# Optimization experiments

Hardware: AMD Instinct MI355X
Metric: run time of the kernel (lower is better)

The kernel has to match this reference:

```python
import jax, jax.numpy as jnp
import numpy as np

B, S, N, HID = 4, 512, 128, 64


def setup_inputs() -> dict:
    key = jax.random.key(0)
    ks = jax.random.split(key, 32)
    def rn(k, shape, scale=0.1):
        return jax.random.normal(k, shape, dtype=jnp.float32) * scale
    adj = jax.random.randint(ks[0], (N, N), 0, 2).astype(jnp.int32)
    adj = adj.at[jnp.arange(N), jnp.arange(N)].set(1)  # self loops
    inp = {
        'x': jax.random.normal(ks[1], (B, S, N, 1), dtype=jnp.float32),
        'adj': adj,
        'emb_w': rn(ks[2], (1, 16)), 'emb_b': jnp.zeros((16,), jnp.float32),
        'gat1_W': rn(ks[3], (16, 16)), 'gat1_a': rn(ks[4], (32, 1)),
        'gat2_W': rn(ks[5], (16, 8)), 'gat2_a': rn(ks[6], (16, 1)),
        'Wih0': rn(ks[7], (4 * HID, N)), 'Whh0': rn(ks[8], (4 * HID, HID)),
        'bih0': jnp.zeros((4 * HID,), jnp.float32), 'bhh0': jnp.zeros((4 * HID,), jnp.float32),
        'Wih1': rn(ks[9], (4 * HID, HID)), 'Whh1': rn(ks[10], (4 * HID, HID)),
        'bih1': jnp.zeros((4 * HID,), jnp.float32), 'bhh1': jnp.zeros((4 * HID,), jnp.float32),
    }
    comb = HID + 8 * N
    for i, name in enumerate(['dir', 'ret', 'vol']):
        o = 2 if name == 'vol' else 1
        inp[name + '_w1'] = rn(ks[11 + 4 * i], (comb, 32))
        inp[name + '_b1'] = jnp.zeros((32,), jnp.float32)
        inp[name + '_w2'] = rn(ks[12 + 4 * i], (32, o))
        inp[name + '_b2'] = jnp.zeros((o,), jnp.float32)
    return inp


def _gat(h, W, a, mask):
    # e_ij = leakyrelu(a1 . Wh_i + a2 . Wh_j): avoid torch's [M,N,N,2F] concat.
    Wh = h @ W                                  # [M, N, F]
    Fo = W.shape[1]
    f1 = Wh @ a[:Fo]                            # [M, N, 1]
    f2 = Wh @ a[Fo:]                            # [M, N, 1]
    e = jax.nn.leaky_relu(f1 + jnp.swapaxes(f2, 1, 2), 0.2)  # [M, N, N]
    e = jnp.where(mask, e, jnp.float32(-9e15))
    attn = jax.nn.softmax(e, axis=2)
    return attn @ Wh                            # [M, N, F]


def _lstm_layer(xs, Wih, Whh, bih, bhh):
    # xs: [S, B, I]; PyTorch gate order i, f, g, o
    Bsz = xs.shape[1]
    Hd = Whh.shape[1]
    def step(carry, xt):
        h, c = carry
        g = xt @ Wih.T + h @ Whh.T + bih + bhh
        i, f, gg, o = jnp.split(g, 4, axis=-1)
        c = jax.nn.sigmoid(f) * c + jax.nn.sigmoid(i) * jnp.tanh(gg)
        h = jax.nn.sigmoid(o) * jnp.tanh(c)
        return (h, c), h
    init = (jnp.zeros((Bsz, Hd), xs.dtype), jnp.zeros((Bsz, Hd), xs.dtype))
    _, hs = jax.lax.scan(step, init, xs)
    return hs


def reference(x, adj, emb_w, emb_b, gat1_W, gat1_a, gat2_W, gat2_a,
              Wih0, Whh0, bih0, bhh0, Wih1, Whh1, bih1, bhh1,
              dir_w1, dir_b1, dir_w2, dir_b2,
              ret_w1, ret_b1, ret_w2, ret_b2,
              vol_w1, vol_b1, vol_w2, vol_b2):
    Bz, Sz, Nz, _ = x.shape
    mask = (adj > 0)[None]                      # [1, N, N], broadcast over B*S
    xe = (x @ emb_w + emb_b).reshape(Bz * Sz, Nz, 16)
    xg = jax.nn.elu(_gat(xe, gat1_W, gat1_a, mask))   # gat1 concat=True -> elu
    xg = _gat(xg, gat2_W, gat2_a, mask)               # gat2 concat=False
    xg_out = xg.reshape(Bz, Sz, Nz * 8)[:, -1, :]
    xs = jnp.swapaxes(x.reshape(Bz, Sz, Nz), 0, 1)    # [S, B, N]
    hs = _lstm_layer(xs, Wih0, Whh0, bih0, bhh0)
    hs = _lstm_layer(hs, Wih1, Whh1, bih1, bhh1)      # inter-layer dropout off (eval)
    xl_out = hs[-1]                                   # [B, 64]
    c = jnp.concatenate([xl_out, xg_out], axis=1)     # [B, 64 + 8N]
    def head(w1, b1, w2, b2):
        return jax.nn.relu(c @ w1 + b1) @ w2 + b2
    return (head(dir_w1, dir_b1, dir_w2, dir_b2),
            head(ret_w1, ret_b1, ret_w2, ret_b2),
            head(vol_w1, vol_b1, vol_w2, vol_b2))
```

## Files before the change

kernel.cpp:

```cpp
#include <hip/hip_runtime.h>

#define SEQ   512
#define BATCH 4
#define NN    128
#define HID   64
#define G4    256
#define MAGIC 0x13579BDF

__device__ __forceinline__ float frcp(float x)  { return __builtin_amdgcn_rcpf(x); }
__device__ __forceinline__ float fsigm(float x) { return frcp(1.f + __expf(-x)); }
__device__ __forceinline__ float ftanh(float x) { return 1.f - 2.f * frcp(1.f + __expf(2.f * x)); }
__device__ __forceinline__ float lrelu(float x) { return x > 0.f ? x : 0.2f * x; }
__device__ __forceinline__ float dot4f(float4 w, float4 h) {
  return fmaf(w.x, h.x, fmaf(w.y, h.y, fmaf(w.z, h.z, w.w * h.w)));
}
__device__ __forceinline__ void pin4(float4& v) {
  asm volatile("" : "+v"(v.x), "+v"(v.y), "+v"(v.z), "+v"(v.w));
}
__device__ __forceinline__ float qsum(float x) {
  x += __int_as_float(__builtin_amdgcn_update_dpp(
      0, __float_as_int(x), 0xB1, 0xF, 0xF, true));
  x += __int_as_float(__builtin_amdgcn_update_dpp(
      0, __float_as_int(x), 0x4E, 0xF, 0xF, true));
  return x;
}
__device__ __forceinline__ float dotacc(const float4* w, const float4* h, float a) {
#pragma unroll
  for (int c = 0; c < 4; ++c) {
    a = fmaf(w[c].x, h[c].x, a);
    a = fmaf(w[c].y, h[c].y, a);
    a = fmaf(w[c].z, h[c].z, a);
    a = fmaf(w[c].w, h[c].w, a);
  }
  return a;
}

#define BAR_LDS() asm volatile("s_waitcnt lgkmcnt(0)\n\ts_barrier" ::: "memory")

__global__ __attribute__((amdgpu_flat_work_group_size(768, 768),
                          amdgpu_waves_per_eu(3, 3)))
void fused_all(
    const float* __restrict__ x, const int* __restrict__ adj,
    const float* __restrict__ emb_w, const float* __restrict__ emb_b,
    const float* __restrict__ W1, const float* __restrict__ a1,
    const float* __restrict__ W2, const float* __restrict__ a2,
    const float* __restrict__ Wih0, const float* __restrict__ Whh0,
    const float* __restrict__ bih0, const float* __restrict__ bhh0,
    const float* __restrict__ Wih1, const float* __restrict__ Whh1,
    const float* __restrict__ bih1, const float* __restrict__ bhh1,
    const float* __restrict__ dw1, const float* __restrict__ db1,
    const float* __restrict__ dw2, const float* __restrict__ db2,
    const float* __restrict__ rw1, const float* __restrict__ rb1,
    const float* __restrict__ rw2, const float* __restrict__ rb2,
    const float* __restrict__ vw1, const float* __restrict__ vb1,
    const float* __restrict__ vw2, const float* __restrict__ vb2,
    float* __restrict__ X0T, float* __restrict__ xg,
    int* __restrict__ flags, float* __restrict__ out)
{
  const int bid = blockIdx.x;
  const int tid = threadIdx.x;

  if (bid >= 4) {
    const int c = bid - 4;
    __shared__ __align__(16) float xls[NN];
    {
      const int g = tid >> 1, half = tid & 1;
      float4 w4[16];
      if (tid < 512) {
        const float4* wp = reinterpret_cast<const float4*>(Wih0 + g * NN + half * 64);
#pragma unroll
        for (int i = 0; i < 16; ++i) w4[i] = wp[i];
#pragma unroll
        for (int i = 0; i < 16; ++i) pin4(w4[i]);
      }
      const float bsum = (tid < 512) ? (bih0[g] + bhh0[g]) : 0.f;
      for (int phase = 0; phase < 4; ++phase) {
        const int T = c + 128 * phase;
        for (int bb = 0; bb < BATCH; ++bb) {
          if (tid < NN) xls[tid] = x[(bb * SEQ + T) * NN + tid];
          __syncthreads();
          if (tid < 512) {
            const float4* hp = reinterpret_cast<const float4*>(&xls[half * 64]);
            float p0 = 0.f, p1 = 0.f, p2 = 0.f, p3 = 0.f;
#pragma unroll
            for (int k = 0; k < 16; k += 4) {
              p0 += dot4f(w4[k],     hp[k]);
              p1 += dot4f(w4[k + 1], hp[k + 1]);
              p2 += dot4f(w4[k + 2], hp[k + 2]);
              p3 += dot4f(w4[k + 3], hp[k + 3]);
            }
            float p = (p0 + p1) + (p2 + p3);
            p += __shfl_xor(p, 1);
            if (half == 0)
              X0T[(4 * T + bb) * G4 + (g & 63) * 4 + (g >> 6)] = p + bsum;
          }
          __syncthreads();
        }
        if (tid == 0 && phase == 0)
          __hip_atomic_store(&flags[c], MAGIC, __ATOMIC_RELEASE,
                             __HIP_MEMORY_SCOPE_AGENT);
        if (tid == 0 && phase == 3)
          __hip_atomic_store(&flags[128 + c], MAGIC, __ATOMIC_RELEASE,
                             __HIP_MEMORY_SCOPE_AGENT);
      }
    }
    if (bid >= 8) return;

    const int b = bid - 4;
    __shared__ float adjm[NN * 129];
    __shared__ __align__(16) float gxls[NN];
    __shared__ float u[16], v[16];
    __shared__ float Wh2[NN][9];
    __shared__ float f1b[NN], f2b[NN];
    __shared__ float p[NN];

    for (int idx = tid; idx < NN * NN; idx += 768)
      adjm[(idx >> 7) * 129 + (idx & 127)] = (adj[idx] > 0) ? 1.f : 0.f;
    if (tid < NN) gxls[tid] = x[(b * SEQ + (SEQ - 1)) * NN + tid];
    if (tid < 16) {
      float uu = 0.f, vv = 0.f;
      for (int fp = 0; fp < 16; ++fp) {
        uu += emb_w[fp] * W1[fp * 16 + tid];
        vv += emb_b[fp] * W1[fp * 16 + tid];
      }
      u[tid] = uu; v[tid] = vv;
    }
    __syncthreads();
    float s1 = 0.f, t1 = 0.f, s2 = 0.f, t2 = 0.f;
    for (int f = 0; f < 16; ++f) {
      s1 += u[f] * a1[f];      t1 += v[f] * a1[f];
      s2 += u[f] * a1[16 + f]; t2 += v[f] * a1[16 + f];
    }
    if (tid < NN) {
      const int i = tid;
      const float f1i = gxls[i] * s1 + t1;
      float m = -1e30f;
      for (int j = 0; j < NN; ++j)
        if (adjm[i * 129 + j] != 0.f)
          m = fmaxf(m, lrelu(f1i + gxls[j] * s2 + t2));
      float ssum = 0.f, ps = 0.f;
      for (int j = 0; j < NN; ++j)
        if (adjm[i * 129 + j] != 0.f) {
          const float wgt = __expf(lrelu(f1i + gxls[j] * s2 + t2) - m);
          ssum += wgt; ps += wgt * gxls[j];
        }
      p[i] = ps / ssum;
    }
    __syncthreads();
    if (tid < NN) {
      const int i = tid;
      float xg1[16];
#pragma unroll
      for (int f = 0; f < 16; ++f) {
        const float ov = p[i] * u[f] + v[f];
        xg1[f] = ov > 0.f ? ov : expm1f(ov);
      }
      float wrow[8];
#pragma unroll
      for (int f2 = 0; f2 < 8; ++f2) wrow[f2] = 0.f;
#pragma unroll
      for (int f = 0; f < 16; ++f) {
        const float xv = xg1[f];
#pragma unroll
        for (int f2 = 0; f2 < 8; ++f2) wrow[f2] += xv * W2[f * 8 + f2];
      }
      float fb1 = 0.f, fb2 = 0.f;
#pragma unroll
      for (int f2 = 0; f2 < 8; ++f2) {
        Wh2[i][f2] = wrow[f2];
        fb1 += wrow[f2] * a2[f2];
        fb2 += wrow[f2] * a2[8 + f2];
      }
      f1b[i] = fb1; f2b[i] = fb2;
    }
    __syncthreads();
    if (tid < NN) {
      const int i = tid;
      const float fi = f1b[i];
      float m = -1e30f;
      for (int j = 0; j < NN; ++j)
        if (adjm[i * 129 + j] != 0.f)
          m = fmaxf(m, lrelu(fi + f2b[j]));
      float ssum = 0.f;
      float o[8];
#pragma unroll
      for (int f2 = 0; f2 < 8; ++f2) o[f2] = 0.f;
      for (int j = 0; j < NN; ++j)
        if (adjm[i * 129 + j] != 0.f) {
          const float wgt = __expf(lrelu(fi + f2b[j]) - m);
          ssum += wgt;
#pragma unroll
          for (int f2 = 0; f2 < 8; ++f2) o[f2] += wgt * Wh2[j][f2];
        }
      const float inv = 1.f / ssum;
#pragma unroll
      for (int f2 = 0; f2 < 8; ++f2)
        xg[b * (NN * 8) + i * 8 + f2] = o[f2] * inv;
    }
    __syncthreads();
    if (tid == 0)
      __hip_atomic_store(&flags[256 + b], MAGIC, __ATOMIC_RELEASE,
                         __HIP_MEMORY_SCOPE_AGENT);
    return;
  }

  const int b   = bid;
  const int t   = tid;
  const int grp = t >> 8;
  const int r   = t & 255;
  const int uu  = r >> 2, q2 = r & 3;

  __shared__ __align__(16) float hb[2][2][HID];
  __shared__ __align__(16) float P1[2][G4];
  __shared__ float cbuf[1088];
  __shared__ float hidc[96];

  const float* Wsrc = (grp == 0) ? Whh0 : (grp == 1) ? Wih1 : Whh1;
  float4 w[4][4];
#pragma unroll
  for (int j = 0; j < 4; ++j) {
    const int row = (uu + 64 * j) * HID + 16 * q2;
#pragma unroll
    for (int c = 0; c < 4; ++c)
      w[j][c] = *reinterpret_cast<const float4*>(Wsrc + row + 4 * c);
  }
  float4 b1v = make_float4(0.f, 0.f, 0.f, 0.f);
  if (grp == 2) {
    b1v.x = bih1[uu]       + bhh1[uu];
    b1v.y = bih1[uu + 64]  + bhh1[uu + 64];
    b1v.z = bih1[uu + 128] + bhh1[uu + 128];
    b1v.w = bih1[uu + 192] + bhh1[uu + 192];
  }

  if (t < 256) reinterpret_cast<float*>(hb)[t] = 0.f;
  float cst = 0.f;
  const float* X0b = X0T + b * G4 + uu * 4;

  int c_ok;
  {
    if (t < 32) {
      while (__hip_atomic_fetch_add(&flags[t], 0, __ATOMIC_ACQUIRE,
                                    __HIP_MEMORY_SCOPE_AGENT) != MAGIC) {}
    }
    __syncthreads();
    c_ok = 31;
  }

  const float4* hpA = reinterpret_cast<const float4*>(
      (grp == 2) ? &hb[0][1][0] : &hb[0][0][0]) + 4 * q2;
  const float4* hpB = reinterpret_cast<const float4*>(
      (grp == 2) ? &hb[1][1][0] : &hb[1][0][0]) + 4 * q2;

  float4 xa0 = make_float4(0.f, 0.f, 0.f, 0.f), xa1 = xa0, xa2 = xa0, xa3 = xa0;
  if (grp == 0) {
    xa0 = *reinterpret_cast<const float4*>(X0b + 0 * (BATCH * G4));
    xa1 = *reinterpret_cast<const float4*>(X0b + 1 * (BATCH * G4));
    xa2 = *reinterpret_cast<const float4*>(X0b + 2 * (BATCH * G4));
    xa3 = *reinterpret_cast<const float4*>(X0b + 3 * (BATCH * G4));
  }

#define LSTM_STEP(TT, RB, WB, XV)                                              \
  do {                                                                         \
    const float4* hp = (RB) ? hpB : hpA;                                       \
    float4 hq[4];                                                              \
    hq[0] = hp[0]; hq[1] = hp[1]; hq[2] = hp[2]; hq[3] = hp[3];                \
    float4 p1v = make_float4(0.f, 0.f, 0.f, 0.f);                              \
    if (grp == 2) p1v = *reinterpret_cast<const float4*>(&P1[1 - (RB)][uu * 4]); \
    const float A0 = dotacc(w[0], hq, 0.f);                                    \
    const float A1 = dotacc(w[1], hq, 0.f);                                    \
    const float A2 = dotacc(w[2], hq, 0.f);                                    \
    const float A3 = dotacc(w[3], hq, 0.f);                                    \
    const float S0 = qsum(A0), S1 = qsum(A1), S2 = qsum(A2), S3 = qsum(A3);    \
    if (grp == 0) {                                                            \
      if ((TT) < SEQ) {                                                        \
        const float gi = fsigm(S0 + (XV).x);                                   \
        const float gf = fsigm(S1 + (XV).y);                                   \
        const float gg = ftanh(S2 + (XV).z);                                   \
        const float go = fsigm(S3 + (XV).w);                                   \
        cst = fmaf(gf, cst, gi * gg);                                          \
        if (q2 == 0) hb[WB][0][uu] = go * ftanh(cst);                          \
      }                                                                        \
    } else if (grp == 1) {                                                     \
      if ((TT) >= 1 && (TT) <= SEQ) {                                          \
        const float sel = (q2 == 0) ? S0 : (q2 == 1) ? S1 : (q2 == 2) ? S2 : S3; \
        P1[RB][r] = sel;                                                       \
      }                                                                        \
    } else {                                                                   \
      if ((TT) >= 2) {                                                         \
        const float gi = fsigm(S0 + p1v.x + b1v.x);                            \
        const float gf = fsigm(S1 + p1v.y + b1v.y);                            \
        const float gg = ftanh(S2 + p1v.z + b1v.z);                            \
        const float go = fsigm(S3 + p1v.w + b1v.w);                            \
        cst = fmaf(gf, cst, gi * gg);                                          \
        if (q2 == 0) hb[WB][1][uu] = go * ftanh(cst);                          \
      }                                                                        \
    }                                                                          \
    BAR_LDS();                                                                 \
  } while (0)

  for (int tt = 0; tt < SEQ; tt += 4) {
    if (tt + 36 > c_ok && c_ok < 255) {
      const int base = c_ok + 1;
      if (t < 32 && base + t <= 255) {
        while (__hip_atomic_fetch_add(&flags[base + t], 0, __ATOMIC_ACQUIRE,
                                      __HIP_MEMORY_SCOPE_AGENT) != MAGIC) {}
      }
      __syncthreads();
      c_ok = (base + 31 < 255) ? base + 31 : 255;
    }
#pragma unroll
    for (int j = 0; j < 4; ++j) {
      pin4(w[j][0]); pin4(w[j][1]); pin4(w[j][2]); pin4(w[j][3]);
    }
    float4 xb0 = xa0, xb1 = xa1, xb2 = xa2, xb3 = xa3;
    if (grp == 0 && tt + 4 < SEQ) {
      xb0 = *reinterpret_cast<const float4*>(X0b + (tt + 4) * (BATCH * G4));
      xb1 = *reinterpret_cast<const float4*>(X0b + (tt + 5) * (BATCH * G4));
      xb2 = *reinterpret_cast<const float4*>(X0b + (tt + 6) * (BATCH * G4));
      xb3 = *reinterpret_cast<const float4*>(X0b + (tt + 7) * (BATCH * G4));
    }
    LSTM_STEP(tt + 0, 0, 1, xa0);
    LSTM_STEP(tt + 1, 1, 0, xa1);
    LSTM_STEP(tt + 2, 0, 1, xa2);
    LSTM_STEP(tt + 3, 1, 0, xa3);
    xa0 = xb0; xa1 = xb1; xa2 = xb2; xa3 = xb3;
  }
  LSTM_STEP(512, 0, 1, xa0);
  LSTM_STEP(513, 1, 0, xa1);
#undef LSTM_STEP

  if (t == 0) {
    while (__hip_atomic_fetch_add(&flags[256 + b], 0, __ATOMIC_ACQUIRE,
                                  __HIP_MEMORY_SCOPE_AGENT) != MAGIC) {}
  }
  __syncthreads();

  if (t < 64) cbuf[t] = hb[0][1][t];
  for (int k = t; k < 1024; k += 768) cbuf[64 + k] = xg[b * 1024 + k];
  __syncthreads();
  if (t < 96) {
    const int head = t >> 5, h = t & 31;
    const float* w1 = (head == 0) ? dw1 : (head == 1) ? rw1 : vw1;
    const float* b1 = (head == 0) ? db1 : (head == 1) ? rb1 : vb1;
    float a0 = 0.f, a1v = 0.f, a2v = 0.f, a3v = 0.f;
    for (int k = 0; k < 1088; k += 4) {
      a0  = fmaf(cbuf[k],     w1[k * 32 + h],       a0);
      a1v = fmaf(cbuf[k + 1], w1[(k + 1) * 32 + h], a1v);
      a2v = fmaf(cbuf[k + 2], w1[(k + 2) * 32 + h], a2v);
      a3v = fmaf(cbuf[k + 3], w1[(k + 3) * 32 + h], a3v);
    }
    hidc[head * 32 + h] = fmaxf(b1[h] + ((a0 + a1v) + (a2v + a3v)), 0.f);
  }
  __syncthreads();
  if (t < 4) {
    const int head2 = (t < 2) ? t : 2;
    const int o = (t < 2) ? 0 : (t - 2);
    const int odim = (t < 2) ? 1 : 2;
    const float* w2  = (head2 == 0) ? dw2 : (head2 == 1) ? rw2 : vw2;
    const float* b2p = (head2 == 0) ? db2 : (head2 == 1) ? rb2 : vb2;
    float acc = b2p[o];
    for (int hh = 0; hh < 32; ++hh)
      acc = fmaf(hidc[head2 * 32 + hh], w2[hh * odim + o], acc);
    const int off = (t == 0) ? b : (t == 1) ? (4 + b) : (8 + 2 * b + o);
    out[off] = acc;
  }
}

extern "C" void kernel_launch(void* const* d_in, const int* in_sizes, int n_in,
                              void* d_out, int out_size, void* d_ws, size_t ws_size,
                              hipStream_t stream) {
  const float* x     = (const float*)d_in[0];
  const int*   adj   = (const int*)  d_in[1];
  const float* emb_w = (const float*)d_in[2];
  const float* emb_b = (const float*)d_in[3];
  const float* g1W   = (const float*)d_in[4];
  const float* g1a   = (const float*)d_in[5];
  const float* g2W   = (const float*)d_in[6];
  const float* g2a   = (const float*)d_in[7];
  const float* Wih0  = (const float*)d_in[8];
  const float* Whh0  = (const float*)d_in[9];
  const float* bih0  = (const float*)d_in[10];
  const float* bhh0  = (const float*)d_in[11];
  const float* Wih1  = (const float*)d_in[12];
  const float* Whh1  = (const float*)d_in[13];
  const float* bih1  = (const float*)d_in[14];
  const float* bhh1  = (const float*)d_in[15];
  const float* dw1 = (const float*)d_in[16]; const float* db1 = (const float*)d_in[17];
  const float* dw2 = (const float*)d_in[18]; const float* db2 = (const float*)d_in[19];
  const float* rw1 = (const float*)d_in[20]; const float* rb1 = (const float*)d_in[21];
  const float* rw2 = (const float*)d_in[22]; const float* rb2 = (const float*)d_in[23];
  const float* vw1 = (const float*)d_in[24]; const float* vb1 = (const float*)d_in[25];
  const float* vw2 = (const float*)d_in[26]; const float* vb2 = (const float*)d_in[27];

  float* ws = (float*)d_ws;
  float* X0 = ws;
  float* xg = ws + SEQ * BATCH * G4;
  int*  flg = (int*)(xg + BATCH * NN * 8);
  float* out = (float*)d_out;

  hipLaunchKernelGGL(fused_all, dim3(132), dim3(768), 0, stream,
                     x, adj, emb_w, emb_b, g1W, g1a, g2W, g2a,
                     Wih0, Whh0, bih0, bhh0, Wih1, Whh1, bih1, bhh1,
                     dw1, db1, dw2, db2, rw1, rb1, rw2, rb2,
                     vw1, vb1, vw2, vb2,
                     X0, xg, flg, out);
}
```

Measured before the change: 425.2 us.

## Store LSTM recurrent weights and hidden state in fp16 and use dot2 instructions

Converts the register-resident LSTM weight tiles and the shared hidden-state buffers from fp32 to packed fp16. The recurrent matvec then uses v_dot2_f32_f16, which halves the FMA count, the LDS read volume and the weight register footprint. Hidden values are packed in pairs through a DPP lane shuffle before the store. This shortens the serial per-step critical path of the recurrence, at the cost of fp16 rounding of weights and hidden state, which may affect accuracy.

```diff
diff --git a/kernel.cpp b/kernel.cpp
--- a/kernel.cpp
+++ b/kernel.cpp
@@ -7,6 +7,8 @@
 #define G4    256
 #define MAGIC 0x13579BDF
 
+typedef _Float16 half2v __attribute__((ext_vector_type(2)));
+
 __device__ __forceinline__ float frcp(float x)  { return __builtin_amdgcn_rcpf(x); }
 __device__ __forceinline__ float fsigm(float x) { return frcp(1.f + __expf(-x)); }
 __device__ __forceinline__ float ftanh(float x) { return 1.f - 2.f * frcp(1.f + __expf(2.f * x)); }
@@ -24,15 +26,32 @@
       0, __float_as_int(x), 0x4E, 0xF, 0xF, true));
   return x;
 }
-__device__ __forceinline__ float dotacc(const float4* w, const float4* h, float a) {
-#pragma unroll
-  for (int c = 0; c < 4; ++c) {
-    a = fmaf(w[c].x, h[c].x, a);
-    a = fmaf(w[c].y, h[c].y, a);
-    a = fmaf(w[c].z, h[c].z, a);
-    a = fmaf(w[c].w, h[c].w, a);
-  }
-  return a;
+__device__ __forceinline__ half2v u2h(unsigned u) {
+  return __builtin_bit_cast(half2v, u);
+}
+__device__ __forceinline__ half2v pk16(float lo, float hi) {
+  return __builtin_bit_cast(half2v, __builtin_amdgcn_cvt_pkrtz(lo, hi));
+}
+__device__ __forceinline__ float fdot2(half2v a, half2v b, float c) {
+#if __has_builtin(__builtin_amdgcn_fdot2)
+  return __builtin_amdgcn_fdot2(a, b, c, false);
+#else
+  float d = c;
+  asm("v_dot2_f32_f16 %0, %1, %2, %0" : "+v"(d) : "v"(a), "v"(b));
+  return d;
+#endif
+}
+__device__ __forceinline__ float dot8h(const half2v* w, const uint4& a,
+                                       const uint4& b, float acc) {
+  acc = fdot2(w[0], u2h(a.x), acc);
+  acc = fdot2(w[1], u2h(a.y), acc);
+  acc = fdot2(w[2], u2h(a.z), acc);
+  acc = fdot2(w[3], u2h(a.w), acc);
+  acc = fdot2(w[4], u2h(b.x), acc);
+  acc = fdot2(w[5], u2h(b.y), acc);
+  acc = fdot2(w[6], u2h(b.z), acc);
+  acc = fdot2(w[7], u2h(b.w), acc);
+  return acc;
 }
 
 #define BAR_LDS() asm volatile("s_waitcnt lgkmcnt(0)\n\ts_barrier" ::: "memory")
@@ -210,19 +229,22 @@
   const int r   = t & 255;
   const int uu  = r >> 2, q2 = r & 3;
 
-  __shared__ __align__(16) float hb[2][2][HID];
+  __shared__ __align__(16) half2v hb16[2][2][HID / 2];
   __shared__ __align__(16) float P1[2][G4];
   __shared__ float cbuf[1088];
   __shared__ float hidc[96];
 
   const float* Wsrc = (grp == 0) ? Whh0 : (grp == 1) ? Wih1 : Whh1;
-  float4 w[4][4];
+  half2v w16[4][8];
 #pragma unroll
   for (int j = 0; j < 4; ++j) {
-    const int row = (uu + 64 * j) * HID + 16 * q2;
-#pragma unroll
-    for (int c = 0; c < 4; ++c)
-      w[j][c] = *reinterpret_cast<const float4*>(Wsrc + row + 4 * c);
+    const float* wr = Wsrc + (uu + 64 * j) * HID + 16 * q2;
+#pragma unroll
+    for (int c = 0; c < 4; ++c) {
+      const float4 wv = *reinterpret_cast<const float4*>(wr + 4 * c);
+      w16[j][2 * c]     = half2v{(_Float16)wv.x, (_Float16)wv.y};
+      w16[j][2 * c + 1] = half2v{(_Float16)wv.z, (_Float16)wv.w};
+    }
   }
   float4 b1v = make_float4(0.f, 0.f, 0.f, 0.f);
   if (grp == 2) {
@@ -232,7 +254,7 @@
     b1v.w = bih1[uu + 192] + bhh1[uu + 192];
   }
 
-  if (t < 256) reinterpret_cast<float*>(hb)[t] = 0.f;
+  if (t < 128) reinterpret_cast<unsigned*>(hb16)[t] = 0u;
   float cst = 0.f;
   const float* X0b = X0T + b * G4 + uu * 4;
 
@@ -246,10 +268,9 @@
     c_ok = 31;
   }
 
-  const float4* hpA = reinterpret_cast<const float4*>(
-      (grp == 2) ? &hb[0][1][0] : &hb[0][0][0]) + 4 * q2;
-  const float4* hpB = reinterpret_cast<const float4*>(
-      (grp == 2) ? &hb[1][1][0] : &hb[1][0][0]) + 4 * q2;
+  const int lay = (grp == 2) ? 1 : 0;
+  const uint4* hpA = reinterpret_cast<const uint4*>(&hb16[0][lay][0]) + 2 * q2;
+  const uint4* hpB = reinterpret_cast<const uint4*>(&hb16[1][lay][0]) + 2 * q2;
 
   float4 xa0 = make_float4(0.f, 0.f, 0.f, 0.f), xa1 = xa0, xa2 = xa0, xa3 = xa0;
   if (grp == 0) {
@@ -259,17 +280,25 @@
     xa3 = *reinterpret_cast<const float4*>(X0b + 3 * (BATCH * G4));
   }
 
+#define PACK_WRITE(LAYER, WB, HV)                                              \
+  do {                                                                         \
+    const float pr_ = __int_as_float(__builtin_amdgcn_update_dpp(              \
+        0, __float_as_int(HV), 0x141, 0xF, 0xF, true));                        \
+    if ((r & 7) == 0)                                                          \
+      hb16[WB][LAYER][r >> 3] = pk16((HV), pr_);                               \
+  } while (0)
+
 #define LSTM_STEP(TT, RB, WB, XV)                                              \
   do {                                                                         \
-    const float4* hp = (RB) ? hpB : hpA;                                       \
-    float4 hq[4];                                                              \
-    hq[0] = hp[0]; hq[1] = hp[1]; hq[2] = hp[2]; hq[3] = hp[3];                \
+    const uint4* hp = (RB) ? hpB : hpA;                                        \
+    const uint4 ua = hp[0];                                                    \
+    const uint4 ub = hp[1];                                                    \
     float4 p1v = make_float4(0.f, 0.f, 0.f, 0.f);                              \
     if (grp == 2) p1v = *reinterpret_cast<const float4*>(&P1[1 - (RB)][uu * 4]); \
-    const float A0 = dotacc(w[0], hq, 0.f);                                    \
-    const float A1 = dotacc(w[1], hq, 0.f);                                    \
-    const float A2 = dotacc(w[2], hq, 0.f);                                    \
-    const float A3 = dotacc(w[3], hq, 0.f);                                    \
+    const float A0 = dot8h(w16[0], ua, ub, 0.f);                               \
+    const float A1 = dot8h(w16[1], ua, ub, 0.f);                               \
+    const float A2 = dot8h(w16[2], ua, ub, 0.f);                               \
+    const float A3 = dot8h(w16[3], ua, ub, 0.f);                               \
     const float S0 = qsum(A0), S1 = qsum(A1), S2 = qsum(A2), S3 = qsum(A3);    \
     if (grp == 0) {                                                            \
       if ((TT) < SEQ) {                                                        \
@@ -278,7 +307,8 @@
         const float gg = ftanh(S2 + (XV).z);                                   \
         const float go = fsigm(S3 + (XV).w);                                   \
         cst = fmaf(gf, cst, gi * gg);                                          \
-        if (q2 == 0) hb[WB][0][uu] = go * ftanh(cst);                          \
+        const float hv = go * ftanh(cst);                                      \
+        PACK_WRITE(0, WB, hv);                                                 \
       }                                                                        \
     } else if (grp == 1) {                                                     \
       if ((TT) >= 1 && (TT) <= SEQ) {                                          \
@@ -292,7 +322,8 @@
         const float gg = ftanh(S2 + p1v.z + b1v.z);                            \
         const float go = fsigm(S3 + p1v.w + b1v.w);                            \
         cst = fmaf(gf, cst, gi * gg);                                          \
-        if (q2 == 0) hb[WB][1][uu] = go * ftanh(cst);                          \
+        const float hv = go * ftanh(cst);                                      \
+        PACK_WRITE(1, WB, hv);                                                 \
       }                                                                        \
     }                                                                          \
     BAR_LDS();                                                                 \
@@ -310,7 +341,9 @@
     }
 #pragma unroll
     for (int j = 0; j < 4; ++j) {
-      pin4(w[j][0]); pin4(w[j][1]); pin4(w[j][2]); pin4(w[j][3]);
+      asm volatile("" : "+v"(w16[j][0]), "+v"(w16[j][1]), "+v"(w16[j][2]),
+                        "+v"(w16[j][3]), "+v"(w16[j][4]), "+v"(w16[j][5]),
+                        "+v"(w16[j][6]), "+v"(w16[j][7]));
     }
     float4 xb0 = xa0, xb1 = xa1, xb2 = xa2, xb3 = xa3;
     if (grp == 0 && tt + 4 < SEQ) {
@@ -328,6 +361,7 @@
   LSTM_STEP(512, 0, 1, xa0);
   LSTM_STEP(513, 1, 0, xa1);
 #undef LSTM_STEP
+#undef PACK_WRITE
 
   if (t == 0) {
     while (__hip_atomic_fetch_add(&flags[256 + b], 0, __ATOMIC_ACQUIRE,
@@ -335,7 +369,10 @@
   }
   __syncthreads();
 
-  if (t < 64) cbuf[t] = hb[0][1][t];
+  if (t < 64) {
+    const _Float16* hh = reinterpret_cast<const _Float16*>(&hb16[0][1][0]);
+    cbuf[t] = (float)hh[t];
+  }
   for (int k = t; k < 1024; k += 768) cbuf[64 + k] = xg[b * 1024 + k];
   __syncthreads();
   if (t < 96) {
```

Result: slower. 445.4 us (+4.7%).
